# Kernel optimization log

Hardware: AMD Instinct MI355X
Metric: run time of the kernel (lower is better)

## Reference

```python
import jax, jax.numpy as jnp
import numpy as np

N = 50000          # nodes
E = 800000         # edges (avg in-degree 16)
NFEAT, F = 128, 64 # input feat, hidden width (outfeat = outd_1 = outd_2 = 64)
ALPHA = 0.2        # leaky relu slope
AVG_LIN = 16.0             # sum(bin*hist)/N for deg histogram (all deg 16)
AVG_LOG = float(np.log(17.0))  # sum(log(bin+1)*hist)/N


def setup_inputs():
    key = jax.random.key(0)
    ks = jax.random.split(key, 16)
    g = lambda i, shp, s: (jax.random.normal(ks[i], shp, jnp.float32) * s)
    return {
        "x": g(0, (N, NFEAT), 1.0),
        "adj": jnp.zeros((1,), jnp.float32),
        "edge_index": jax.random.randint(ks[1], (2, E), 0, N, dtype=jnp.int32),
        "W0": g(2, (NFEAT, F), NFEAT ** -0.5), "b0": jnp.zeros((F,), jnp.float32),
        "c1_pre_W": g(3, (2 * F, F), (2 * F) ** -0.5), "c1_pre_b": jnp.zeros((F,), jnp.float32),
        "c1_post_W": g(4, (5 * F, F), (5 * F) ** -0.5), "c1_post_b": jnp.zeros((F,), jnp.float32),
        "c1_lin_W": g(5, (F, F), F ** -0.5), "c1_lin_b": jnp.zeros((F,), jnp.float32),
        "c2_pre_W": g(6, (2 * F, F), (2 * F) ** -0.5), "c2_pre_b": jnp.zeros((F,), jnp.float32),
        "c2_post_W": g(7, (5 * F, F), (5 * F) ** -0.5), "c2_post_b": jnp.zeros((F,), jnp.float32),
        "c2_lin_W": g(8, (F, F), F ** -0.5), "c2_lin_b": jnp.zeros((F,), jnp.float32),
        "W2": g(9, (F, 1), F ** -0.5), "b2": jnp.zeros((1,), jnp.float32),
    }


def pna_conv(x, src, dst, pre_W, pre_b, post_W, post_b, lin_W, lin_b):
    # message: pre_nn(cat[x_i, x_j]) per edge  (x_i = target, x_j = source)
    h = jnp.concatenate([x[dst], x[src]], axis=-1) @ pre_W + pre_b  # [E, F]
    cnt = jax.ops.segment_sum(jnp.ones((h.shape[0],), h.dtype), dst, num_segments=N)
    deg = jnp.clip(cnt, 1.0)                                        # [N]
    mean = jax.ops.segment_sum(h, dst, num_segments=N) / deg[:, None]
    mx = jax.ops.segment_max(h, dst, num_segments=N)
    mx = jnp.where(cnt[:, None] > 0, mx, 0.0)                       # empty segs -> 0
    agg = jnp.concatenate([mean, mx], axis=-1)                      # [N, 2F]
    att = agg * (AVG_LOG / jnp.log(deg + 1.0))[:, None]             # attenuation scaler
    lin = agg * (deg / AVG_LIN)[:, None]                            # linear scaler
    out = jnp.concatenate([x, att, lin], axis=-1)                   # [N, 5F]
    out = out @ post_W + post_b
    return out @ lin_W + lin_b


def reference(x, adj, edge_index, W0, b0,
              c1_pre_W, c1_pre_b, c1_post_W, c1_post_b, c1_lin_W, c1_lin_b,
              c2_pre_W, c2_pre_b, c2_post_W, c2_post_b, c2_lin_W, c2_lin_b,
              W2, b2):
    src, dst = edge_index[0], edge_index[1]
    h = jax.nn.leaky_relu(x @ W0 + b0, negative_slope=ALPHA)  # dropout = id (eval)
    h = jax.nn.relu(pna_conv(h, src, dst, c1_pre_W, c1_pre_b, c1_post_W, c1_post_b, c1_lin_W, c1_lin_b))
    h = jax.nn.relu(pna_conv(h, src, dst, c2_pre_W, c2_pre_b, c2_post_W, c2_post_b, c2_lin_W, c2_lin_b))
    return h @ W2 + b2  # [N, 1]
```

## Files before the change

kernel.cpp:

```cpp
#include <hip/hip_runtime.h>
#include <hip/hip_bf16.h>

typedef __hip_bfloat16 bf16;
typedef unsigned short u16;
typedef unsigned int u32;
typedef __attribute__((ext_vector_type(8))) short short8;
typedef __attribute__((ext_vector_type(4))) float f32x4;

static constexpr float AVG_LOG_C = 2.8332133440562162f;
#define BCAP 1024
#define CHUNK 2048
#define PREP_TOTAL (8192 + 20480 * 2 + 64 * 5 + 1)

__device__ __forceinline__ u32 f2bf_bits(float f) {
    u32 u = __float_as_uint(f);
    return (u + 0x7fffu + ((u >> 16) & 1u)) >> 16;
}
__device__ __forceinline__ float bf2f(u16 b) {
    return __uint_as_float(((u32)b) << 16);
}

__device__ __forceinline__ bool block_detect(const u32* __restrict__ xwords,
                                             int* sflag, int tid) {
    if (tid < 64) {
        int good = 0;
        for (int i = tid; i < 2048; i += 64) {
            u32 lo = xwords[i] & 0xffffu;
            float v = __uint_as_float(lo << 16);
            float a = fabsf(v);
            if (v == 0.0f || (a >= 1e-3f && a <= 100.0f)) good++;
        }
        for (int off = 32; off; off >>= 1) good += __shfl_xor(good, off, 64);
        if (tid == 0) *sflag = (2 * good > 2048) ? 1 : 0;
    }
    __syncthreads();
    return *sflag != 0;
}

__device__ __forceinline__ short8 load_bfrag_raw(const void* __restrict__ W, bool isbf,
                                                 int kk0, int col) {
    short8 r;
    if (isbf) {
        const u16* p = (const u16*)W + (size_t)kk0 * 64 + col;
#pragma unroll
        for (int j = 0; j < 8; ++j) r[j] = (short)p[j * 64];
    } else {
        const float* p = (const float*)W + (size_t)kk0 * 64 + col;
#pragma unroll
        for (int j = 0; j < 8; ++j) r[j] = (short)f2bf_bits(p[j * 64]);
    }
    return r;
}

__global__ __launch_bounds__(512, 4) void k1_kernel(
    const void* __restrict__ xraw,
    const int* __restrict__ srcs, const int* __restrict__ dsts,
    int* __restrict__ bcnt, u32* __restrict__ bstage,
    const void* __restrict__ W0r,  const void* __restrict__ b0r,
    const void* __restrict__ pre1r, const void* __restrict__ preb1r,
    const void* __restrict__ post1r, const void* __restrict__ postb1r,
    const void* __restrict__ lin1r, const void* __restrict__ linb1r,
    const void* __restrict__ pre2r, const void* __restrict__ preb2r,
    const void* __restrict__ post2r, const void* __restrict__ postb2r,
    const void* __restrict__ lin2r, const void* __restrict__ linb2r,
    const void* __restrict__ W2r,  const void* __restrict__ b2r,
    u16* __restrict__ pre2p, u16* __restrict__ wf1p, u16* __restrict__ wf2p,
    float* __restrict__ bfo1, float* __restrict__ bfo2,
    float* __restrict__ preb1f, float* __restrict__ preb2f,
    float* __restrict__ W2f, float* __restrict__ b2f, int* __restrict__ flag,
    u16* __restrict__ hA, u16* __restrict__ PQ,
    int n, int e, int nb, int gB, int scatB) {
    __shared__ union {
        struct { int lhist[2048]; int lbase[2048]; } sc;
        struct { __align__(16) u16 xsh[32 * 136]; __align__(16) u16 hsh[32 * 72]; } gx;
    } sm;
    __shared__ int sflag;
    int tid = threadIdx.x;
    int bx = (int)blockIdx.x;

    if (bx < gB) {
        int wave = __builtin_amdgcn_readfirstlane(tid >> 6);
        int lane = tid & 63;
        int blockbase = bx * 32;
        bool isbf = block_detect((const u32*)xraw, &sflag, tid);
        {
            int row = tid >> 4;
            int cgx = (tid & 15) * 8;
            int grow = blockbase + row;
            short8 v = short8{0, 0, 0, 0, 0, 0, 0, 0};
            if (grow < n) {
                if (isbf) {
                    v = *(const short8*)((const u16*)xraw + (size_t)grow * 128 + cgx);
                } else {
                    const float* xf = (const float*)xraw + (size_t)grow * 128 + cgx;
                    f32x4 a0 = *(const f32x4*)xf;
                    f32x4 a1 = *(const f32x4*)(xf + 4);
#pragma unroll
                    for (int j = 0; j < 4; ++j) {
                        v[j]     = (short)f2bf_bits(a0[j]);
                        v[4 + j] = (short)f2bf_bits(a1[j]);
                    }
                }
            }
            *(short8*)&sm.gx.xsh[row * 136 + cgx] = v;
        }
        __syncthreads();
        int rt = wave & 1, ct = wave >> 1;
        int arl = rt * 16 + (lane & 15);
        int koff = (lane >> 4) * 8;
        int colh = ct * 16 + (lane & 15);
        f32x4 acc = f32x4{0.f, 0.f, 0.f, 0.f};
#pragma unroll
        for (int s = 0; s < 4; ++s) {
            short8 a = *(const short8*)&sm.gx.xsh[arl * 136 + s * 32 + koff];
            short8 b = load_bfrag_raw(W0r, isbf, s * 32 + (lane >> 4) * 8, colh);
            acc = __builtin_amdgcn_mfma_f32_16x16x32_bf16(a, b, acc, 0, 0, 0);
        }
        {
            float bv = isbf ? bf2f(((const u16*)b0r)[colh]) : ((const float*)b0r)[colh];
            int r0l = rt * 16 + (lane >> 4) * 4;
#pragma unroll
            for (int r = 0; r < 4; ++r) {
                float v = acc[r] + bv;
                v = v > 0.f ? v : 0.2f * v;
                u16 bits = (u16)f2bf_bits(v);
                sm.gx.hsh[(r0l + r) * 72 + colh] = bits;
                int grow = blockbase + r0l + r;
                if (grow < n) hA[(size_t)grow * 64 + colh] = bits;
            }
        }
        __syncthreads();
#pragma unroll
        for (int half = 0; half < 2; ++half) {
            int tile = wave * 2 + half;
            int rt2 = tile & 1, ct2 = tile >> 1;
            int ar2 = rt2 * 16 + (lane & 15);
            int col128 = ct2 * 16 + (lane & 15);
            int colw = col128 & 63;
            int radd = (col128 < 64) ? 0 : 64;
            f32x4 acc2 = f32x4{0.f, 0.f, 0.f, 0.f};
#pragma unroll
            for (int s = 0; s < 2; ++s) {
                short8 a = *(const short8*)&sm.gx.hsh[ar2 * 72 + s * 32 + koff];
                short8 b = load_bfrag_raw(pre1r, isbf,
                                          s * 32 + (lane >> 4) * 8 + radd, colw);
                acc2 = __builtin_amdgcn_mfma_f32_16x16x32_bf16(a, b, acc2, 0, 0, 0);
            }
            int r02 = rt2 * 16 + (lane >> 4) * 4;
#pragma unroll
            for (int r = 0; r < 4; ++r) {
                int grow = blockbase + r02 + r;
                if (grow < n) PQ[(size_t)grow * 128 + col128] = (u16)f2bf_bits(acc2[r]);
            }
        }
        return;
    }

    if (bx < gB + scatB) {
        int cbase = (bx - gB) * CHUNK;
        for (int bb = tid; bb < nb; bb += 512) sm.sc.lhist[bb] = 0;
        __syncthreads();
#pragma unroll
        for (int i = 0; i < CHUNK; i += 512) {
            int e0 = cbase + i + tid;
            if (e0 < e) atomicAdd(&sm.sc.lhist[dsts[e0] >> 5], 1);
        }
        __syncthreads();
        for (int bb = tid; bb < nb; bb += 512) {
            int c = sm.sc.lhist[bb];
            sm.sc.lbase[bb] = c ? atomicAdd(&bcnt[bb], c) : 0;
            sm.sc.lhist[bb] = 0;
        }
        __syncthreads();
#pragma unroll
        for (int i = 0; i < CHUNK; i += 512) {
            int e0 = cbase + i + tid;
            if (e0 < e) {
                int d = dsts[e0];
                int bb = d >> 5;
                int pos = sm.sc.lbase[bb] + atomicAdd(&sm.sc.lhist[bb], 1);
                if (pos < BCAP)
                    bstage[(size_t)bb * BCAP + pos] = (u32)srcs[e0] | ((u32)(d & 31) << 17);
            }
        }
        return;
    }

    bool isbf = block_detect((const u32*)xraw, &sflag, tid);
    if (bx == gB + scatB && tid == 0) *flag = sflag;
    auto ld = [&](const void* p, int i) -> float {
        return isbf ? bf2f(((const u16*)p)[i]) : ((const float*)p)[i];
    };
    int idx = (bx - gB - scatB) * 512 + tid;
    if (idx < 8192) {
        int j = idx & 7, l = (idx >> 3) & 63, tt = idx >> 9;
        int c = tt & 7, s = tt >> 3;
        int kk = s * 32 + (l >> 4) * 8 + j;
        int col = c * 16 + (l & 15);
        float v = (col < 64) ? ld(pre2r, kk * 64 + col)
                             : ld(pre2r, (64 + kk) * 64 + (col - 64));
        pre2p[idx] = (u16)f2bf_bits(v);
        return;
    }
    idx -= 8192;
    for (int which = 0; which < 2; ++which) {
        if (idx < 20480) {
            const void* postW = which ? post2r : post1r;
            const void* linW  = which ? lin2r  : lin1r;
            u16* dst = which ? wf2p : wf1p;
            int j = idx & 7, l = (idx >> 3) & 63, tt = idx >> 9;
            int c = tt & 3, s = tt >> 2;
            int kk = s * 32 + (l >> 4) * 8 + j;
            int col = c * 16 + (l & 15);
            float a = 0.f;
            for (int k = 0; k < 64; ++k)
                a = fmaf(ld(postW, kk * 64 + k), ld(linW, k * 64 + col), a);
            dst[idx] = (u16)f2bf_bits(a);
            return;
        }
        idx -= 20480;
    }
    for (int which = 0; which < 2; ++which) {
        if (idx < 64) {
            const void* postb = which ? postb2r : postb1r;
            const void* linW  = which ? lin2r : lin1r;
            const void* linb  = which ? linb2r : linb1r;
            float* dst = which ? bfo2 : bfo1;
            float a = ld(linb, idx);
            for (int k = 0; k < 64; ++k)
                a = fmaf(ld(postb, k), ld(linW, k * 64 + idx), a);
            dst[idx] = a;
            return;
        }
        idx -= 64;
    }
    if (idx < 64) { preb1f[idx] = ld(preb1r, idx); return; }
    idx -= 64;
    if (idx < 64) { preb2f[idx] = ld(preb2r, idx); return; }
    idx -= 64;
    if (idx < 64) { W2f[idx] = ld(W2r, idx); return; }
    idx -= 64;
    if (idx < 1) { b2f[0] = ld(b2r, 0); }
}

template<int FINAL>
__global__ __launch_bounds__(512, 4) void agg_gemm_kernel(
    const u16* __restrict__ PQ, const u16* __restrict__ h,
    const u32* __restrict__ bstage, const int* __restrict__ bcnt,
    const float* __restrict__ prebf, const u16* __restrict__ Wfp,
    const float* __restrict__ bfo, const u16* __restrict__ prenextp,
    u16* __restrict__ hout, u16* __restrict__ PQout,
    const float* __restrict__ W2f, const float* __restrict__ b2f,
    void* __restrict__ out, const int* __restrict__ flag, int n) {
    constexpr int PAD = 328;
    __shared__ __align__(16) u16 vsh[32 * PAD];
    __shared__ __align__(16) u16 hsh[32 * 72];
    __shared__ u32 lel[BCAP];
    __shared__ int loff[32], lcnt[32], lcur[32];
    __shared__ float fsum[32];
    int tid = threadIdx.x;
    int wave = __builtin_amdgcn_readfirstlane(tid >> 6);
    int lane = tid & 63;
    int b = blockIdx.x;
    int blockbase = b * 32;
    float pbl = prebf[lane];
    if (tid < 32) { lcnt[tid] = 0; if (FINAL) fsum[tid] = 0.f; }
    __syncthreads();
    int cb = min(bcnt[b], BCAP);
    const u32* st = bstage + (size_t)b * BCAP;
    for (int i = tid; i < cb; i += 512) atomicAdd(&lcnt[st[i] >> 17], 1);
    __syncthreads();
    if (wave == 0) {
        int c = (lane < 32) ? lcnt[lane] : 0;
        int s = c;
        for (int off = 1; off < 32; off <<= 1) {
            int t = __shfl_up(s, (unsigned)off, 64);
            if (lane >= off) s += t;
        }
        if (lane < 32) {
            loff[lane] = s - c;
            lcur[lane] = s - c;
        }
    }
    __syncthreads();
    for (int i = tid; i < cb; i += 512) {
        u32 e = st[i];
        int pos = atomicAdd(&lcur[e >> 17], 1);
        lel[pos] = (e & 0x1ffffu) << 8;
    }
    __syncthreads();
    const char* PQc = (const char*)PQ;
    u32 voffb = 128u + 2u * (u32)lane;
#pragma unroll
    for (int t = 0; t < 4; ++t) {
        int nl = wave * 4 + t;
        int node = blockbase + nl;
        u16* vrow = &vsh[nl * PAD];
        if (node < n) {
            int beg = loff[nl], end = beg + lcnt[nl];
            int cnt = end - beg;
            float s = 0.f, m = -3.4e38f;
            int e = beg;
            for (; e + 8 <= end; e += 8) {
                float q0 = bf2f(*(const u16*)(PQc + lel[e]     + voffb));
                float q1 = bf2f(*(const u16*)(PQc + lel[e + 1] + voffb));
                float q2 = bf2f(*(const u16*)(PQc + lel[e + 2] + voffb));
                float q3 = bf2f(*(const u16*)(PQc + lel[e + 3] + voffb));
                float q4 = bf2f(*(const u16*)(PQc + lel[e + 4] + voffb));
                float q5 = bf2f(*(const u16*)(PQc + lel[e + 5] + voffb));
                float q6 = bf2f(*(const u16*)(PQc + lel[e + 6] + voffb));
                float q7 = bf2f(*(const u16*)(PQc + lel[e + 7] + voffb));
                s += ((q0 + q1) + (q2 + q3)) + ((q4 + q5) + (q6 + q7));
                m = fmaxf(m, fmaxf(fmaxf(fmaxf(q0, q1), fmaxf(q2, q3)),
                                   fmaxf(fmaxf(q4, q5), fmaxf(q6, q7))));
            }
            for (; e + 4 <= end; e += 4) {
                float q0 = bf2f(*(const u16*)(PQc + lel[e]     + voffb));
                float q1 = bf2f(*(const u16*)(PQc + lel[e + 1] + voffb));
                float q2 = bf2f(*(const u16*)(PQc + lel[e + 2] + voffb));
                float q3 = bf2f(*(const u16*)(PQc + lel[e + 3] + voffb));
                s += (q0 + q1) + (q2 + q3);
                m = fmaxf(fmaxf(m, fmaxf(q0, q1)), fmaxf(q2, q3));
            }
            for (; e < end; ++e) {
                float q = bf2f(*(const u16*)(PQc + lel[e] + voffb));
                s += q;
                m = fmaxf(m, q);
            }
            float mean, mx, deg;
            if (cnt > 0) {
                deg = (float)cnt;
                float p = bf2f(PQ[(size_t)node * 128 + lane]) + pbl;
                mean = p + s / deg;
                mx = p + m;
            } else {
                deg = 1.f; mean = 0.f; mx = 0.f;
            }
            float att = AVG_LOG_C / logf(deg + 1.f);
            float lin = deg * (1.f / 16.f);
            vrow[lane]       = h[(size_t)node * 64 + lane];
            vrow[64 + lane]  = (u16)f2bf_bits(att * mean);
            vrow[128 + lane] = (u16)f2bf_bits(att * mx);
            vrow[192 + lane] = (u16)f2bf_bits(lin * mean);
            vrow[256 + lane] = (u16)f2bf_bits(lin * mx);
        } else {
            vrow[lane] = 0; vrow[64 + lane] = 0; vrow[128 + lane] = 0;
            vrow[192 + lane] = 0; vrow[256 + lane] = 0;
        }
    }
    __syncthreads();
    int rt = wave & 1, ct = wave >> 1;
    int arl = rt * 16 + (lane & 15);
    int koff = (lane >> 4) * 8;
    f32x4 acc = f32x4{0.f, 0.f, 0.f, 0.f};
#pragma unroll
    for (int s = 0; s < 10; ++s) {
        short8 a = *(const short8*)&vsh[arl * PAD + s * 32 + koff];
        short8 b2 = *(const short8*)(Wfp + ((size_t)(s * 4 + ct) * 64 + lane) * 8);
        acc = __builtin_amdgcn_mfma_f32_16x16x32_bf16(a, b2, acc, 0, 0, 0);
    }
    int col = ct * 16 + (lane & 15);
    float bv = bfo[col];
    int r0l = rt * 16 + (lane >> 4) * 4;
    if constexpr (!FINAL) {
#pragma unroll
        for (int r = 0; r < 4; ++r) {
            float v = fmaxf(acc[r] + bv, 0.f);
            u16 bits = (u16)f2bf_bits(v);
            hsh[(r0l + r) * 72 + col] = bits;
            int grow = blockbase + r0l + r;
            if (grow < n) hout[(size_t)grow * 64 + col] = bits;
        }
        __syncthreads();
#pragma unroll
        for (int half = 0; half < 2; ++half) {
            int tile = wave * 2 + half;
            int rt2 = tile & 1, ct2 = tile >> 1;
            int ar2 = rt2 * 16 + (lane & 15);
            f32x4 acc2 = f32x4{0.f, 0.f, 0.f, 0.f};
#pragma unroll
            for (int s = 0; s < 2; ++s) {
                short8 a = *(const short8*)&hsh[ar2 * 72 + s * 32 + koff];
                short8 b2 = *(const short8*)(prenextp + ((size_t)(s * 8 + ct2) * 64 + lane) * 8);
                acc2 = __builtin_amdgcn_mfma_f32_16x16x32_bf16(a, b2, acc2, 0, 0, 0);
            }
            int col2 = ct2 * 16 + (lane & 15);
            int r02 = rt2 * 16 + (lane >> 4) * 4;
#pragma unroll
            for (int r = 0; r < 4; ++r) {
                int grow = blockbase + r02 + r;
                if (grow < n) PQout[(size_t)grow * 128 + col2] = (u16)f2bf_bits(acc2[r]);
            }
        }
    } else {
        float w2 = W2f[col];
        float part[4];
#pragma unroll
        for (int r = 0; r < 4; ++r)
            part[r] = fmaxf(acc[r] + bv, 0.f) * w2;
#pragma unroll
        for (int r = 0; r < 4; ++r) {
            float v = part[r];
            v += __shfl_xor(v, 1, 64);
            v += __shfl_xor(v, 2, 64);
            v += __shfl_xor(v, 4, 64);
            v += __shfl_xor(v, 8, 64);
            if ((lane & 15) == 0) atomicAdd(&fsum[r0l + r], v);
        }
        __syncthreads();
        if (tid < 32) {
            int grow = blockbase + tid;
            if (grow < n) {
                float res = fsum[tid] + b2f[0];
                if (*flag) ((u16*)out)[grow] = (u16)f2bf_bits(res);
                else       ((float*)out)[grow] = res;
            }
        }
    }
}

extern "C" void kernel_launch(void* const* d_in, const int* in_sizes, int n_in,
                              void* d_out, int out_size, void* d_ws, size_t ws_size,
                              hipStream_t stream) {
    const int N = in_sizes[0] / 128;
    const int E = in_sizes[2] / 2;
    const int nb = (N + 31) >> 5;
    const int* ei = (const int*)d_in[2];
    const int* esrc = ei;
    const int* edst = ei + E;

    char* w = (char*)d_ws;
    auto alloc = [&](size_t bytes) -> void* {
        void* p = (void*)w;
        w += (bytes + 255) & ~(size_t)255;
        return p;
    };
    int* flag    = (int*)alloc(4);
    int* bcnt    = (int*)alloc((size_t)nb * 4);
    u32* bstage  = (u32*)alloc((size_t)nb * BCAP * 4);
    u16* pre2p   = (u16*)alloc(64 * 128 * 2);
    u16* wf1p    = (u16*)alloc(320 * 64 * 2);
    u16* wf2p    = (u16*)alloc(320 * 64 * 2);
    float* bfo1  = (float*)alloc(64 * 4);
    float* bfo2  = (float*)alloc(64 * 4);
    float* preb1f= (float*)alloc(64 * 4);
    float* preb2f= (float*)alloc(64 * 4);
    float* W2f   = (float*)alloc(64 * 4);
    float* b2f_  = (float*)alloc(4);
    u16* hA      = (u16*)alloc((size_t)N * 64 * 2);
    u16* hB      = (u16*)alloc((size_t)N * 64 * 2);
    u16* PQA     = (u16*)alloc((size_t)N * 128 * 2);
    u16* PQB     = (u16*)alloc((size_t)N * 128 * 2);

    hipMemsetAsync(bcnt, 0, (size_t)nb * 4, stream);

    int gB = (N + 31) / 32;
    int scatB = (E + CHUNK - 1) / CHUNK;
    int prepB = (PREP_TOTAL + 511) / 512;
    k1_kernel<<<gB + scatB + prepB, 512, 0, stream>>>(
        d_in[0], esrc, edst, bcnt, bstage,
        d_in[3], d_in[4], d_in[5], d_in[6], d_in[7], d_in[8], d_in[9], d_in[10],
        d_in[11], d_in[12], d_in[13], d_in[14], d_in[15], d_in[16], d_in[17], d_in[18],
        pre2p, wf1p, wf2p, bfo1, bfo2, preb1f, preb2f, W2f, b2f_, flag,
        hA, PQA, N, E, nb, gB, scatB);

    agg_gemm_kernel<0><<<gB, 512, 0, stream>>>(
        PQA, hA, bstage, bcnt, preb1f, wf1p, bfo1, pre2p, hB, PQB,
        nullptr, nullptr, nullptr, flag, N);

    agg_gemm_kernel<1><<<gB, 512, 0, stream>>>(
        PQB, hB, bstage, bcnt, preb2f, wf2p, bfo2, nullptr, nullptr, nullptr,
        W2f, b2f_, d_out, flag, N);
}
```

Before: 206.4 us.

## Replace bucketed edge staging with per-node fixed-capacity adjacency lists and prepack weights

Edges are now scattered straight into per-node slots (capacity 64) with a global atomic per destination, replacing the two-pass per-block histogram and bucket staging. This removes the in-block counting, prefix scan and local scatter from the aggregation kernels. A new pre-kernel detects the dtype once, zeroes the counters and prepacks W0/pre1 into MFMA fragment order so the GEMM blocks do vector loads instead of strided converted loads. The cost is one global atomic per edge, a larger staging buffer, and silent truncation for nodes with more than 64 in-edges.

New measurement: 243.1 us. 17.8% more time.

```diff
diff --git a/kernel.cpp b/kernel.cpp
--- a/kernel.cpp
+++ b/kernel.cpp
@@ -1,16 +1,14 @@
 #include <hip/hip_runtime.h>
 #include <hip/hip_bf16.h>
 
-typedef __hip_bfloat16 bf16;
 typedef unsigned short u16;
 typedef unsigned int u32;
 typedef __attribute__((ext_vector_type(8))) short short8;
 typedef __attribute__((ext_vector_type(4))) float f32x4;
 
 static constexpr float AVG_LOG_C = 2.8332133440562162f;
-#define BCAP 1024
-#define CHUNK 2048
-#define PREP_TOTAL (8192 + 20480 * 2 + 64 * 5 + 1)
+#define NCAP 64
+#define SCATB 512
 
 __device__ __forceinline__ u32 f2bf_bits(float f) {
     u32 u = __float_as_uint(f);
@@ -37,44 +35,85 @@
     return *sflag != 0;
 }
 
-__device__ __forceinline__ short8 load_bfrag_raw(const void* __restrict__ W, bool isbf,
-                                                 int kk0, int col) {
-    short8 r;
-    if (isbf) {
-        const u16* p = (const u16*)W + (size_t)kk0 * 64 + col;
-#pragma unroll
-        for (int j = 0; j < 8; ++j) r[j] = (short)p[j * 64];
-    } else {
-        const float* p = (const float*)W + (size_t)kk0 * 64 + col;
-#pragma unroll
-        for (int j = 0; j < 8; ++j) r[j] = (short)f2bf_bits(p[j * 64]);
-    }
-    return r;
+__global__ __launch_bounds__(512) void k0_kernel(
+    const u32* __restrict__ xwords, int* __restrict__ flag, int* __restrict__ ncnt,
+    const void* __restrict__ W0r, const void* __restrict__ b0r,
+    const void* __restrict__ pre1r, const void* __restrict__ preb1r,
+    const void* __restrict__ preb2r, const void* __restrict__ W2r,
+    const void* __restrict__ b2r,
+    u16* __restrict__ W0p, u16* __restrict__ pre1p,
+    float* __restrict__ b0f, float* __restrict__ preb1f,
+    float* __restrict__ preb2f, float* __restrict__ W2f, float* __restrict__ b2f,
+    int n, int zB) {
+    __shared__ int sflag;
+    int tid = threadIdx.x;
+    int bx = (int)blockIdx.x;
+    if (bx == 0) {
+        bool v = block_detect(xwords, &sflag, tid);
+        if (tid == 0) *flag = v ? 1 : 0;
+        return;
+    }
+    bx -= 1;
+    if (bx < zB) {
+        int i = bx * 512 + tid;
+        if (i < n) ncnt[i] = 0;
+        return;
+    }
+    bx -= zB;
+    bool isbf = block_detect(xwords, &sflag, tid);
+    auto ld = [&](const void* p, int i) -> float {
+        return isbf ? bf2f(((const u16*)p)[i]) : ((const float*)p)[i];
+    };
+    int idx = bx * 512 + tid;
+    if (idx < 8192) {
+        int j = idx & 7, l = (idx >> 3) & 63, tt = idx >> 9;
+        int c = tt & 3, s = tt >> 2;
+        int kk = s * 32 + (l >> 4) * 8 + j;
+        int col = c * 16 + (l & 15);
+        W0p[idx] = (u16)f2bf_bits(ld(W0r, kk * 64 + col));
+        return;
+    }
+    idx -= 8192;
+    if (idx < 8192) {
+        int j = idx & 7, l = (idx >> 3) & 63, tt = idx >> 9;
+        int c = tt & 7, s = tt >> 3;
+        int kk = s * 32 + (l >> 4) * 8 + j;
+        int col = c * 16 + (l & 15);
+        float v = (col < 64) ? ld(pre1r, kk * 64 + col)
+                             : ld(pre1r, (64 + kk) * 64 + (col - 64));
+        pre1p[idx] = (u16)f2bf_bits(v);
+        return;
+    }
+    idx -= 8192;
+    if (idx < 64) { b0f[idx] = ld(b0r, idx); return; }
+    idx -= 64;
+    if (idx < 64) { preb1f[idx] = ld(preb1r, idx); return; }
+    idx -= 64;
+    if (idx < 64) { preb2f[idx] = ld(preb2r, idx); return; }
+    idx -= 64;
+    if (idx < 64) { W2f[idx] = ld(W2r, idx); return; }
+    idx -= 64;
+    if (idx < 1) { b2f[0] = ld(b2r, 0); }
 }
 
 __global__ __launch_bounds__(512, 4) void k1_kernel(
     const void* __restrict__ xraw,
     const int* __restrict__ srcs, const int* __restrict__ dsts,
-    int* __restrict__ bcnt, u32* __restrict__ bstage,
-    const void* __restrict__ W0r,  const void* __restrict__ b0r,
-    const void* __restrict__ pre1r, const void* __restrict__ preb1r,
+    int* __restrict__ ncnt, int* __restrict__ nstage,
+    const u16* __restrict__ W0p, const u16* __restrict__ pre1p,
+    const float* __restrict__ b0f,
+    const void* __restrict__ pre2r,
     const void* __restrict__ post1r, const void* __restrict__ postb1r,
     const void* __restrict__ lin1r, const void* __restrict__ linb1r,
-    const void* __restrict__ pre2r, const void* __restrict__ preb2r,
     const void* __restrict__ post2r, const void* __restrict__ postb2r,
     const void* __restrict__ lin2r, const void* __restrict__ linb2r,
-    const void* __restrict__ W2r,  const void* __restrict__ b2r,
     u16* __restrict__ pre2p, u16* __restrict__ wf1p, u16* __restrict__ wf2p,
     float* __restrict__ bfo1, float* __restrict__ bfo2,
-    float* __restrict__ preb1f, float* __restrict__ preb2f,
-    float* __restrict__ W2f, float* __restrict__ b2f, int* __restrict__ flag,
+    const int* __restrict__ flag,
     u16* __restrict__ hA, u16* __restrict__ PQ,
-    int n, int e, int nb, int gB, int scatB) {
-    __shared__ union {
-        struct { int lhist[2048]; int lbase[2048]; } sc;
-        struct { __align__(16) u16 xsh[32 * 136]; __align__(16) u16 hsh[32 * 72]; } gx;
-    } sm;
-    __shared__ int sflag;
+    int n, int e, int gB) {
+    __shared__ __align__(16) u16 xsh[32 * 136];
+    __shared__ __align__(16) u16 hsh[32 * 72];
     int tid = threadIdx.x;
     int bx = (int)blockIdx.x;
 
@@ -82,7 +121,7 @@
         int wave = __builtin_amdgcn_readfirstlane(tid >> 6);
         int lane = tid & 63;
         int blockbase = bx * 32;
-        bool isbf = block_detect((const u32*)xraw, &sflag, tid);
+        bool isbf = (*flag) != 0;
         {
             int row = tid >> 4;
             int cgx = (tid & 15) * 8;
@@ -102,31 +141,31 @@
                     }
                 }
             }
-            *(short8*)&sm.gx.xsh[row * 136 + cgx] = v;
+            *(short8*)&xsh[row * 136 + cgx] = v;
         }
         __syncthreads();
         int rt = wave & 1, ct = wave >> 1;
         int arl = rt * 16 + (lane & 15);
         int koff = (lane >> 4) * 8;
-        int colh = ct * 16 + (lane & 15);
         f32x4 acc = f32x4{0.f, 0.f, 0.f, 0.f};
 #pragma unroll
         for (int s = 0; s < 4; ++s) {
-            short8 a = *(const short8*)&sm.gx.xsh[arl * 136 + s * 32 + koff];
-            short8 b = load_bfrag_raw(W0r, isbf, s * 32 + (lane >> 4) * 8, colh);
+            short8 a = *(const short8*)&xsh[arl * 136 + s * 32 + koff];
+            short8 b = *(const short8*)(W0p + ((size_t)(s * 4 + ct) * 64 + lane) * 8);
             acc = __builtin_amdgcn_mfma_f32_16x16x32_bf16(a, b, acc, 0, 0, 0);
         }
         {
-            float bv = isbf ? bf2f(((const u16*)b0r)[colh]) : ((const float*)b0r)[colh];
+            int col = ct * 16 + (lane & 15);
+            float bv = b0f[col];
             int r0l = rt * 16 + (lane >> 4) * 4;
 #pragma unroll
             for (int r = 0; r < 4; ++r) {
                 float v = acc[r] + bv;
                 v = v > 0.f ? v : 0.2f * v;
                 u16 bits = (u16)f2bf_bits(v);
-                sm.gx.hsh[(r0l + r) * 72 + colh] = bits;
+                hsh[(r0l + r) * 72 + col] = bits;
                 int grow = blockbase + r0l + r;
-                if (grow < n) hA[(size_t)grow * 64 + colh] = bits;
+                if (grow < n) hA[(size_t)grow * 64 + col] = bits;
             }
         }
         __syncthreads();
@@ -135,63 +174,41 @@
             int tile = wave * 2 + half;
             int rt2 = tile & 1, ct2 = tile >> 1;
             int ar2 = rt2 * 16 + (lane & 15);
-            int col128 = ct2 * 16 + (lane & 15);
-            int colw = col128 & 63;
-            int radd = (col128 < 64) ? 0 : 64;
             f32x4 acc2 = f32x4{0.f, 0.f, 0.f, 0.f};
 #pragma unroll
             for (int s = 0; s < 2; ++s) {
-                short8 a = *(const short8*)&sm.gx.hsh[ar2 * 72 + s * 32 + koff];
-                short8 b = load_bfrag_raw(pre1r, isbf,
-                                          s * 32 + (lane >> 4) * 8 + radd, colw);
+                short8 a = *(const short8*)&hsh[ar2 * 72 + s * 32 + koff];
+                short8 b = *(const short8*)(pre1p + ((size_t)(s * 8 + ct2) * 64 + lane) * 8);
                 acc2 = __builtin_amdgcn_mfma_f32_16x16x32_bf16(a, b, acc2, 0, 0, 0);
             }
+            int col2 = ct2 * 16 + (lane & 15);
             int r02 = rt2 * 16 + (lane >> 4) * 4;
 #pragma unroll
             for (int r = 0; r < 4; ++r) {
                 int grow = blockbase + r02 + r;
-                if (grow < n) PQ[(size_t)grow * 128 + col128] = (u16)f2bf_bits(acc2[r]);
-            }
-        }
-        return;
-    }
-
-    if (bx < gB + scatB) {
-        int cbase = (bx - gB) * CHUNK;
-        for (int bb = tid; bb < nb; bb += 512) sm.sc.lhist[bb] = 0;
-        __syncthreads();
-#pragma unroll
-        for (int i = 0; i < CHUNK; i += 512) {
-            int e0 = cbase + i + tid;
-            if (e0 < e) atomicAdd(&sm.sc.lhist[dsts[e0] >> 5], 1);
-        }
-        __syncthreads();
-        for (int bb = tid; bb < nb; bb += 512) {
-            int c = sm.sc.lhist[bb];
-            sm.sc.lbase[bb] = c ? atomicAdd(&bcnt[bb], c) : 0;
-            sm.sc.lhist[bb] = 0;
-        }
-        __syncthreads();
-#pragma unroll
-        for (int i = 0; i < CHUNK; i += 512) {
-            int e0 = cbase + i + tid;
-            if (e0 < e) {
-                int d = dsts[e0];
-                int bb = d >> 5;
-                int pos = sm.sc.lbase[bb] + atomicAdd(&sm.sc.lhist[bb], 1);
-                if (pos < BCAP)
-                    bstage[(size_t)bb * BCAP + pos] = (u32)srcs[e0] | ((u32)(d & 31) << 17);
-            }
-        }
-        return;
-    }
-
-    bool isbf = block_detect((const u32*)xraw, &sflag, tid);
-    if (bx == gB + scatB && tid == 0) *flag = sflag;
+                if (grow < n) PQ[(size_t)grow * 128 + col2] = (u16)f2bf_bits(acc2[r]);
+            }
+        }
+        return;
+    }
+    bx -= gB;
+
+    if (bx < SCATB) {
+        int stride = SCATB * 512;
+        for (int i = bx * 512 + tid; i < e; i += stride) {
+            int d = dsts[i];
+            int pos = atomicAdd(&ncnt[d], 1);
+            if (pos < NCAP) nstage[(size_t)d * NCAP + pos] = srcs[i];
+        }
+        return;
+    }
+    bx -= SCATB;
+
+    bool isbf = (*flag) != 0;
     auto ld = [&](const void* p, int i) -> float {
         return isbf ? bf2f(((const u16*)p)[i]) : ((const float*)p)[i];
     };
-    int idx = (bx - gB - scatB) * 512 + tid;
+    int idx = bx * 512 + tid;
     if (idx < 8192) {
         int j = idx & 7, l = (idx >> 3) & 63, tt = idx >> 9;
         int c = tt & 7, s = tt >> 3;
@@ -213,8 +230,19 @@
             int kk = s * 32 + (l >> 4) * 8 + j;
             int col = c * 16 + (l & 15);
             float a = 0.f;
-            for (int k = 0; k < 64; ++k)
-                a = fmaf(ld(postW, kk * 64 + k), ld(linW, k * 64 + col), a);
+            if (isbf) {
+                const u16* pw = (const u16*)postW + (size_t)kk * 64;
+                const u16* lw = (const u16*)linW + col;
+#pragma unroll 8
+                for (int k = 0; k < 64; ++k)
+                    a = fmaf(bf2f(pw[k]), bf2f(lw[(size_t)k * 64]), a);
+            } else {
+                const float* pw = (const float*)postW + (size_t)kk * 64;
+                const float* lw = (const float*)linW + col;
+#pragma unroll 8
+                for (int k = 0; k < 64; ++k)
+                    a = fmaf(pw[k], lw[(size_t)k * 64], a);
+            }
             dst[idx] = (u16)f2bf_bits(a);
             return;
         }
@@ -227,26 +255,30 @@
             const void* linb  = which ? linb2r : linb1r;
             float* dst = which ? bfo2 : bfo1;
             float a = ld(linb, idx);
-            for (int k = 0; k < 64; ++k)
-                a = fmaf(ld(postb, k), ld(linW, k * 64 + idx), a);
+            if (isbf) {
+                const u16* pb = (const u16*)postb;
+                const u16* lw = (const u16*)linW + idx;
+#pragma unroll 8
+                for (int k = 0; k < 64; ++k)
+                    a = fmaf(bf2f(pb[k]), bf2f(lw[(size_t)k * 64]), a);
+            } else {
+                const float* pb = (const float*)postb;
+                const float* lw = (const float*)linW + idx;
+#pragma unroll 8
+                for (int k = 0; k < 64; ++k)
+                    a = fmaf(pb[k], lw[(size_t)k * 64], a);
+            }
             dst[idx] = a;
             return;
         }
         idx -= 64;
     }
-    if (idx < 64) { preb1f[idx] = ld(preb1r, idx); return; }
-    idx -= 64;
-    if (idx < 64) { preb2f[idx] = ld(preb2r, idx); return; }
-    idx -= 64;
-    if (idx < 64) { W2f[idx] = ld(W2r, idx); return; }
-    idx -= 64;
-    if (idx < 1) { b2f[0] = ld(b2r, 0); }
 }
 
 template<int FINAL>
 __global__ __launch_bounds__(512, 4) void agg_gemm_kernel(
     const u16* __restrict__ PQ, const u16* __restrict__ h,
-    const u32* __restrict__ bstage, const int* __restrict__ bcnt,
+    const int* __restrict__ nstage, const int* __restrict__ ncnt,
     const float* __restrict__ prebf, const u16* __restrict__ Wfp,
     const float* __restrict__ bfo, const u16* __restrict__ prenextp,
     u16* __restrict__ hout, u16* __restrict__ PQout,
@@ -255,8 +287,8 @@
     constexpr int PAD = 328;
     __shared__ __align__(16) u16 vsh[32 * PAD];
     __shared__ __align__(16) u16 hsh[32 * 72];
-    __shared__ u32 lel[BCAP];
-    __shared__ int loff[32], lcnt[32], lcur[32];
+    __shared__ u32 lel[32 * NCAP];
+    __shared__ int lcnt[32];
     __shared__ float fsum[32];
     int tid = threadIdx.x;
     int wave = __builtin_amdgcn_readfirstlane(tid >> 6);
@@ -264,29 +296,19 @@
     int b = blockIdx.x;
     int blockbase = b * 32;
     float pbl = prebf[lane];
-    if (tid < 32) { lcnt[tid] = 0; if (FINAL) fsum[tid] = 0.f; }
+    if (tid < 32) {
+        int node = blockbase + tid;
+        lcnt[tid] = (node < n) ? ncnt[node] : 0;
+        if (FINAL) fsum[tid] = 0.f;
+    }
     __syncthreads();
-    int cb = min(bcnt[b], BCAP);
-    const u32* st = bstage + (size_t)b * BCAP;
-    for (int i = tid; i < cb; i += 512) atomicAdd(&lcnt[st[i] >> 17], 1);
-    __syncthreads();
-    if (wave == 0) {
-        int c = (lane < 32) ? lcnt[lane] : 0;
-        int s = c;
-        for (int off = 1; off < 32; off <<= 1) {
-            int t = __shfl_up(s, (unsigned)off, 64);
-            if (lane >= off) s += t;
-        }
-        if (lane < 32) {
-            loff[lane] = s - c;
-            lcur[lane] = s - c;
-        }
-    }
-    __syncthreads();
-    for (int i = tid; i < cb; i += 512) {
-        u32 e = st[i];
-        int pos = atomicAdd(&lcur[e >> 17], 1);
-        lel[pos] = (e & 0x1ffffu) << 8;
+#pragma unroll
+    for (int q = 0; q < 4; ++q) {
+        int idx = q * 512 + tid;
+        int nl = idx >> 6, i = idx & 63;
+        int node = blockbase + nl;
+        if (node < n && i < min(lcnt[nl], NCAP))
+            lel[idx] = (u32)nstage[(size_t)node * NCAP + i] << 8;
     }
     __syncthreads();
     const char* PQc = (const char*)PQ;
@@ -297,8 +319,8 @@
         int node = blockbase + nl;
         u16* vrow = &vsh[nl * PAD];
         if (node < n) {
-            int beg = loff[nl], end = beg + lcnt[nl];
-            int cnt = end - beg;
+            int cnt = lcnt[nl];
+            int beg = nl * NCAP, end = beg + min(cnt, NCAP);
             float s = 0.f, m = -3.4e38f;
             int e = beg;
             for (; e + 8 <= end; e += 8) {
@@ -424,7 +446,6 @@
                               hipStream_t stream) {
     const int N = in_sizes[0] / 128;
     const int E = in_sizes[2] / 2;
-    const int nb = (N + 31) >> 5;
     const int* ei = (const int*)d_in[2];
     const int* esrc = ei;
     const int* edst = ei + E;
@@ -436,8 +457,10 @@
         return p;
     };
     int* flag    = (int*)alloc(4);
-    int* bcnt    = (int*)alloc((size_t)nb * 4);
-    u32* bstage  = (u32*)alloc((size_t)nb * BCAP * 4);
+    int* ncnt    = (int*)alloc((size_t)N * 4);
+    int* nstage  = (int*)alloc((size_t)N * NCAP * 4);
+    u16* W0p     = (u16*)alloc(128 * 64 * 2);
+    u16* pre1p   = (u16*)alloc(64 * 128 * 2);
     u16* pre2p   = (u16*)alloc(64 * 128 * 2);
     u16* wf1p    = (u16*)alloc(320 * 64 * 2);
     u16* wf2p    = (u16*)alloc(320 * 64 * 2);
@@ -445,6 +468,7 @@
     float* bfo2  = (float*)alloc(64 * 4);
     float* preb1f= (float*)alloc(64 * 4);
     float* preb2f= (float*)alloc(64 * 4);
+    float* b0f   = (float*)alloc(64 * 4);
     float* W2f   = (float*)alloc(64 * 4);
     float* b2f_  = (float*)alloc(4);
     u16* hA      = (u16*)alloc((size_t)N * 64 * 2);
@@ -452,23 +476,26 @@
     u16* PQA     = (u16*)alloc((size_t)N * 128 * 2);
     u16* PQB     = (u16*)alloc((size_t)N * 128 * 2);
 
-    hipMemsetAsync(bcnt, 0, (size_t)nb * 4, stream);
+    int zB = (N + 511) / 512;
+    k0_kernel<<<1 + zB + 33, 512, 0, stream>>>(
+        (const u32*)d_in[0], flag, ncnt,
+        d_in[3], d_in[4], d_in[5], d_in[6], d_in[12], d_in[17], d_in[18],
+        W0p, pre1p, b0f, preb1f, preb2f, W2f, b2f_, N, zB);
 
     int gB = (N + 31) / 32;
-    int scatB = (E + CHUNK - 1) / CHUNK;
-    int prepB = (PREP_TOTAL + 511) / 512;
-    k1_kernel<<<gB + scatB + prepB, 512, 0, stream>>>(
-        d_in[0], esrc, edst, bcnt, bstage,
-        d_in[3], d_in[4], d_in[5], d_in[6], d_in[7], d_in[8], d_in[9], d_in[10],
-        d_in[11], d_in[12], d_in[13], d_in[14], d_in[15], d_in[16], d_in[17], d_in[18],
-        pre2p, wf1p, wf2p, bfo1, bfo2, preb1f, preb2f, W2f, b2f_, flag,
-        hA, PQA, N, E, nb, gB, scatB);
+    k1_kernel<<<gB + SCATB + 97, 512, 0, stream>>>(
+        d_in[0], esrc, edst, ncnt, nstage,
+        W0p, pre1p, b0f,
+        d_in[11], d_in[7], d_in[8], d_in[9], d_in[10],
+        d_in[13], d_in[14], d_in[15], d_in[16],
+        pre2p, wf1p, wf2p, bfo1, bfo2, flag,
+        hA, PQA, N, E, gB);
 
     agg_gemm_kernel<0><<<gB, 512, 0, stream>>>(
-        PQA, hA, bstage, bcnt, preb1f, wf1p, bfo1, pre2p, hB, PQB,
+        PQA, hA, nstage, ncnt, preb1f, wf1p, bfo1, pre2p, hB, PQB,
         nullptr, nullptr, nullptr, flag, N);
 
     agg_gemm_kernel<1><<<gB, 512, 0, stream>>>(
-        PQB, hB, bstage, bcnt, preb2f, wf2p, bfo2, nullptr, nullptr, nullptr,
+        PQB, hB, nstage, ncnt, preb2f, wf2p, bfo2, nullptr, nullptr, nullptr,
         W2f, b2f_, d_out, flag, N);
 }
```
